# Kernel tuning notes

Hardware: AMD Instinct MI355X
Metric: run time of the kernel (lower is better)

The kernel has to match this reference:

```python
import jax, jax.numpy as jnp
import numpy as np

N_HEAD = 16
D_MODEL = 1024
BATCH = 2
SEQ = 2048


def setup_inputs() -> dict:
    key = jax.random.key(0)
    ks = jax.random.split(key, 12)
    s = 0.02
    inp = {
        "q": jax.random.normal(ks[0], (BATCH, SEQ, D_MODEL), jnp.float32),
        "k": jax.random.normal(ks[1], (BATCH, SEQ, D_MODEL), jnp.float32),
        "v": jax.random.normal(ks[2], (BATCH, SEQ, D_MODEL), jnp.float32),
        "Wq": jax.random.normal(ks[3], (D_MODEL, D_MODEL), jnp.float32) * s,
        "bq": jnp.zeros((D_MODEL,), jnp.float32),
        "Wk": jax.random.normal(ks[4], (D_MODEL, D_MODEL), jnp.float32) * s,
        "bk": jnp.zeros((D_MODEL,), jnp.float32),
        "Wv": jax.random.normal(ks[5], (D_MODEL, D_MODEL), jnp.float32) * s,
        "bv": jnp.zeros((D_MODEL,), jnp.float32),
        "Wo": jax.random.normal(ks[6], (D_MODEL, D_MODEL), jnp.float32) * s,
        "bo": jnp.zeros((D_MODEL,), jnp.float32),
    }
    return inp


def reference(q, k, v, Wq, bq, Wk, bk, Wv, bv, Wo, bo):
    B, S, D = q.shape
    H = N_HEAD
    Dh = D // H
    # NOTE: faithful to source -- scale uses d_model, not head_dim
    scale = D ** 0.5

    # torch nn.Linear: y = x @ W.T + b
    qw = q @ Wq.T + bq
    kw = k @ Wk.T + bk
    vw = v @ Wv.T + bv

    # chunk(n_head, dim=-1) == contiguous last-dim head slices
    qh = qw.reshape(B, S, H, Dh)
    kh = kw.reshape(B, S, H, Dh)
    vh = vw.reshape(B, S, H, Dh)

    scores = jnp.einsum("bshd,bthd->bhst", qh, kh) / scale  # [B,H,S,S]
    causal = jnp.triu(jnp.ones((S, S), dtype=bool), k=1)
    scores = jnp.where(causal, -jnp.inf, scores)
    p = jax.nn.softmax(scores, axis=-1)
    out = jnp.einsum("bhst,bthd->bshd", p, vh).reshape(B, S, D)
    return out @ Wo.T + bo
```

## Files before the change

### kernel.cpp

```cpp
#include <hip/hip_runtime.h>
#include <hip/hip_bf16.h>
#include <stdint.h>
#include <type_traits>

#define NHEAD  16
#define DMODEL 1024
#define BATCH  2
#define SEQ    2048
#define DH     64
#define MROWS  (BATCH*SEQ)

typedef __attribute__((ext_vector_type(8))) short bf16x8;
typedef __attribute__((ext_vector_type(4))) float f32x4;

__device__ inline short f2bs(float f) {
    __hip_bfloat16 h = __float2bfloat16(f);
    return *reinterpret_cast<short*>(&h);
}

__device__ inline uint32_t pk2f(float lo, float hi) {
    uint32_t ul, uh;
    __builtin_memcpy(&ul, &lo, 4);
    __builtin_memcpy(&uh, &hi, 4);
    return __builtin_amdgcn_perm(uh + 0x8000u, ul + 0x8000u, 0x07060302u);
}

__device__ inline float bs2f(short s) {
    const uint32_t u = (uint32_t)(uint16_t)s << 16;
    float f;
    __builtin_memcpy(&f, &u, 4);
    return f;
}

__device__ inline void async16(const void* g, void* l) {
    __builtin_amdgcn_global_load_lds(
        (__attribute__((address_space(1))) void*)g,
        (__attribute__((address_space(3))) void*)l, 16, 0, 0);
}

__global__ __launch_bounds__(256)
void convert_all(const float* __restrict__ Wq, const float* __restrict__ Wk,
                 const float* __restrict__ Wv, const float* __restrict__ Wo,
                 const float* __restrict__ q, const float* __restrict__ k,
                 const float* __restrict__ v,
                 __hip_bfloat16* __restrict__ Wqkv, __hip_bfloat16* __restrict__ Wob,
                 __hip_bfloat16* __restrict__ qb, __hip_bfloat16* __restrict__ kb,
                 __hip_bfloat16* __restrict__ vb)
{
    const int idx = (blockIdx.x * 256 + threadIdx.x) * 8;
    const float* src;
    __hip_bfloat16* dst;
    if (idx < 3 * 1048576) {
        const int g = idx >> 20;
        src = (g == 0 ? Wq : (g == 1 ? Wk : Wv)) + (idx & 1048575);
        dst = Wqkv + idx;
    } else if (idx < 4 * 1048576) {
        src = Wo + (idx - 3 * 1048576);
        dst = Wob + (idx - 3 * 1048576);
    } else if (idx < 8 * 1048576) {
        src = q + (idx - 4 * 1048576);
        dst = qb + (idx - 4 * 1048576);
    } else if (idx < 12 * 1048576) {
        src = k + (idx - 8 * 1048576);
        dst = kb + (idx - 8 * 1048576);
    } else {
        src = v + (idx - 12 * 1048576);
        dst = vb + (idx - 12 * 1048576);
    }
    float4 f0 = *(const float4*)src;
    float4 f1 = *(const float4*)(src + 4);
    short o[8];
    o[0] = f2bs(f0.x); o[1] = f2bs(f0.y); o[2] = f2bs(f0.z); o[3] = f2bs(f0.w);
    o[4] = f2bs(f1.x); o[5] = f2bs(f1.y); o[6] = f2bs(f1.z); o[7] = f2bs(f1.w);
    *(uint4*)dst = *(uint4*)o;
}

template <typename TC, bool DBUF, bool VTOUT>
__global__ __launch_bounds__(256, DBUF ? 2 : 3)
void gemm_bt(const __hip_bfloat16* __restrict__ A0, const __hip_bfloat16* __restrict__ A1,
             const __hip_bfloat16* __restrict__ A2,
             const __hip_bfloat16* __restrict__ B,
             const float* __restrict__ b0, const float* __restrict__ b1, const float* __restrict__ b2,
             TC* __restrict__ C0, TC* __restrict__ C1, TC* __restrict__ C2,
             float os0)
{
    __shared__ short As[DBUF ? 2 : 1][128 * 64];
    __shared__ short Bs[DBUF ? 2 : 1][128 * 64];

    const int t    = threadIdx.x;
    const int lane = t & 63;
    const int w    = t >> 6;
    const int wm   = (w >> 1) * 64;
    const int wn   = (w & 1) * 64;
    const int quad = lane >> 4;
    const int l16  = lane & 15;

    const int g = blockIdx.x >> 3;
    const __hip_bfloat16* A = (g == 0) ? A0 : (g == 1 ? A1 : A2);
    const float* bias       = (g == 0) ? b0 : (g == 1 ? b1 : b2);
    TC* C                   = (g == 0) ? C0 : (g == 1 ? C1 : C2);
    const float osc         = (g == 0) ? os0 : 1.f;
    const int    bm  = blockIdx.y * 128;
    const int    bnl = (blockIdx.x & 7) * 128;
    const size_t bng = (size_t)blockIdx.x * 128;

    f32x4 acc[4][4];
#pragma unroll
    for (int i = 0; i < 4; i++)
#pragma unroll
        for (int j = 0; j < 4; j++)
            acc[i][j] = (f32x4){0.f, 0.f, 0.f, 0.f};

    auto STAGEG = [&](int kt, int buf) {
#pragma unroll
        for (int i = 0; i < 4; i++) {
            const int p  = i * 256 + t;
            const int br = p >> 3;
            const int c8 = ((p & 7) - br) & 7;
            async16(B + (bng + br) * DMODEL + kt + c8 * 8,
                    &Bs[buf][(i * 256 + (w << 6)) * 8]);
            async16(A + (size_t)(bm + br) * DMODEL + kt + c8 * 8,
                    &As[buf][(i * 256 + (w << 6)) * 8]);
        }
    };

    int cur = 0;
    if constexpr (DBUF) STAGEG(0, 0);

    for (int kt = 0; kt < DMODEL; kt += 64) {
        __syncthreads();
        if constexpr (DBUF) {
            if (kt + 64 < DMODEL) STAGEG(kt + 64, cur ^ 1);
        } else {
            STAGEG(kt, 0);
            __syncthreads();
        }

#pragma unroll
        for (int kk = 0; kk < 2; kk++) {
            bf16x8 af[4], bf[4];
#pragma unroll
            for (int mi = 0; mi < 4; mi++) {
                const int row = wm + mi * 16 + l16;
                const int pc  = ((quad + 4 * kk) + row) & 7;
                af[mi] = *(const bf16x8*)&As[cur][row * 64 + pc * 8];
            }
#pragma unroll
            for (int ni = 0; ni < 4; ni++) {
                const int row = wn + ni * 16 + l16;
                const int pc  = ((quad + 4 * kk) + row) & 7;
                bf[ni] = *(const bf16x8*)&Bs[cur][row * 64 + pc * 8];
            }
#pragma unroll
            for (int mi = 0; mi < 4; mi++)
#pragma unroll
                for (int ni = 0; ni < 4; ni++)
                    acc[mi][ni] = __builtin_amdgcn_mfma_f32_16x16x32_bf16(
                        af[mi], bf[ni], acc[mi][ni], 0, 0, 0);
        }
        if constexpr (DBUF) cur ^= 1;
    }

#pragma unroll
    for (int mi = 0; mi < 4; mi++) {
#pragma unroll
        for (int ni = 0; ni < 4; ni++) {
            const int row0 = bm + wm + mi * 16 + quad * 4;
            const int coll = bnl + wn + ni * 16 + l16;
            const float bb = bias[coll];
            if (VTOUT && g == 2) {
                const int hh = coll >> 6, dd = coll & 63;
                const int bb_ = row0 >> 11, s0 = row0 & 2047;
                short o4[4];
#pragma unroll
                for (int r = 0; r < 4; r++) o4[r] = f2bs(acc[mi][ni][r] + bb);
                __hip_bfloat16* dst = (__hip_bfloat16*)C2 +
                    ((size_t)((bb_ * NHEAD + hh) * DH + dd)) * SEQ + s0;
                *(uint2*)dst = *(uint2*)o4;
            } else {
#pragma unroll
                for (int r = 0; r < 4; r++) {
                    const float val = (acc[mi][ni][r] + bb) * osc;
                    if constexpr (std::is_same<TC, float>::value)
                        C[(size_t)(row0 + r) * DMODEL + coll] = val;
                    else
                        C[(size_t)(row0 + r) * DMODEL + coll] = __float2bfloat16(val);
                }
            }
        }
    }
}

__global__ __launch_bounds__(256, 5)
void attn_flash_wg(const __hip_bfloat16* __restrict__ qp,
                   const __hip_bfloat16* __restrict__ kp,
                   const __hip_bfloat16* __restrict__ vt,
                   __hip_bfloat16* __restrict__ po0,
                   __hip_bfloat16* __restrict__ po1,
                   float* __restrict__ ml)
{
    __shared__ short Ks[2][64 * 64];
    __shared__ short Vs[2][64 * 64];

    const int t    = threadIdx.x;
    const int lane = t & 63;
    const int w    = t >> 6;
    const int l16  = lane & 15;
    const int quad = lane >> 4;

    const int bh   = blockIdx.x & 31;
    const int cidx = 79 - ((int)blockIdx.x >> 5);
    int st, c;
    if (cidx < 8)       { st = cidx; c = 0; }
    else if (cidx < 24) { const int u = cidx - 8;  st = 8 + (u >> 1); c = u & 1; }
    else if (cidx < 48) { const int u = cidx - 24; const int q3 = u / 3; st = 16 + q3; c = u - 3 * q3; }
    else                { const int u = cidx - 48; st = 24 + (u >> 2); c = u & 3; }
    const int bid = bh * 80 +
        ((st < 8) ? st : (st < 16) ? 8 + 2 * (st - 8) : (st < 24) ? 24 + 3 * (st - 16)
                                                      : 48 + 4 * (st - 24)) + c;
    const int b = bh >> 4;
    const int h = bh & 15;

    const __hip_bfloat16* qptr =
        qp + (size_t)(b * SEQ + 64 * st + 16 * w + l16) * DMODEL + h * DH + quad * 8;
    bf16x8 aq0 = *(const bf16x8*)qptr;
    bf16x8 aq1 = *(const bf16x8*)(qptr + 32);

    float l = 0.f;
    f32x4 oc[4];
#pragma unroll
    for (int dt = 0; dt < 4; dt++) oc[dt] = (f32x4){0.f, 0.f, 0.f, 0.f};

    const __hip_bfloat16* kbase = kp + (size_t)(b * SEQ) * DMODEL + h * DH;
    const __hip_bfloat16* vbase = vt + (size_t)(bh * DH) * SEQ;

    const int kmax   = 64 * st + 64;
    const int key_lo = 512 * c;
    const int nst    = (min(key_lo + 512, kmax) - key_lo) >> 6;
    const int rql    = 16 * w + l16;

    const int p1  = 256 + t;
    const int r0s = t >> 3,            r1s = p1 >> 3;
    const int c80 = ((t & 7) - r0s) & 7, c81 = ((p1 & 7) - r1s) & 7;
    const int kr0 = (r0s & 3) | ((r0s & 12) << 1) | ((r0s & 16) << 1) | ((r0s & 32) >> 3);
    const int kr1 = (r1s & 3) | ((r1s & 12) << 1) | ((r1s & 16) << 1) | ((r1s & 32) >> 3);
    const __hip_bfloat16* ks0 = kbase + (size_t)(key_lo + kr0) * DMODEL + c80 * 8;
    const __hip_bfloat16* ks1 = kbase + (size_t)(key_lo + kr1) * DMODEL + c81 * 8;
    const __hip_bfloat16* vs0 = vbase + (size_t)r0s * SEQ + key_lo + c80 * 8;
    const __hip_bfloat16* vs1 = vbase + (size_t)r1s * SEQ + key_lo + c81 * 8;

    const int d0 = ((w << 6)) * 8;
    const int d1 = (256 + (w << 6)) * 8;

    async16(ks0, &Ks[0][d0]);
    async16(ks1, &Ks[0][d1]);
    async16(vs0, &Vs[0][d0]);
    async16(vs1, &Vs[0][d1]);
    int cur = 0;
    int key0 = key_lo;

    for (int js = 0; js < nst; ++js) {
        __syncthreads();
        if (js + 1 < nst) {
            ks0 += (size_t)64 * DMODEL;  ks1 += (size_t)64 * DMODEL;
            vs0 += 64;                   vs1 += 64;
            const int nb = cur ^ 1;
            async16(ks0, &Ks[nb][d0]);
            async16(ks1, &Ks[nb][d1]);
            async16(vs0, &Vs[nb][d0]);
            async16(vs1, &Vs[nb][d1]);
        }

        f32x4 sc[4];
        __builtin_amdgcn_s_setprio(1);
#pragma unroll
        for (int ct = 0; ct < 4; ct++) {
            const int row = 16 * ct + l16;
            bf16x8 bk0 = *(const bf16x8*)&Ks[cur][row * 64 + ((quad + row) & 7) * 8];
            bf16x8 bk1 = *(const bf16x8*)&Ks[cur][row * 64 + ((quad + 4 + row) & 7) * 8];
            sc[ct] = __builtin_amdgcn_mfma_f32_16x16x32_bf16(
                bk0, aq0, (f32x4){0.f, 0.f, 0.f, 0.f}, 0, 0, 0);
            sc[ct] = __builtin_amdgcn_mfma_f32_16x16x32_bf16(bk1, aq1, sc[ct], 0, 0, 0);
        }
        __builtin_amdgcn_s_setprio(0);

        if (key0 == 64 * st) {
#pragma unroll
            for (int ct = 0; ct < 4; ct++)
#pragma unroll
                for (int r = 0; r < 4; r++) {
                    const int km = 8 * quad + 32 * (ct & 1) + 4 * (ct >> 1) + r;
                    if (km > rql) sc[ct][r] = -__builtin_inff();
                }
        }

        float psum = 0.f;
#pragma unroll
        for (int ct = 0; ct < 4; ct++)
#pragma unroll
            for (int r = 0; r < 4; r++) {
                const float e = exp2f(sc[ct][r]);
                sc[ct][r] = e;
                psum += e;
            }

        union U8 { uint32_t u[4]; bf16x8 v; } ap0u, ap1u;
        ap0u.u[0] = pk2f(sc[0][0], sc[0][1]);
        ap0u.u[1] = pk2f(sc[0][2], sc[0][3]);
        ap0u.u[2] = pk2f(sc[2][0], sc[2][1]);
        ap0u.u[3] = pk2f(sc[2][2], sc[2][3]);
        ap1u.u[0] = pk2f(sc[1][0], sc[1][1]);
        ap1u.u[1] = pk2f(sc[1][2], sc[1][3]);
        ap1u.u[2] = pk2f(sc[3][0], sc[3][1]);
        ap1u.u[3] = pk2f(sc[3][2], sc[3][3]);

        __builtin_amdgcn_s_setprio(1);
#pragma unroll
        for (int dt = 0; dt < 4; dt++) {
            const int row = 16 * dt + l16;
            bf16x8 bv0 = *(const bf16x8*)&Vs[cur][row * 64 + ((quad + row) & 7) * 8];
            bf16x8 bv1 = *(const bf16x8*)&Vs[cur][row * 64 + ((quad + 4 + row) & 7) * 8];
            oc[dt] = __builtin_amdgcn_mfma_f32_16x16x32_bf16(ap0u.v, bv0, oc[dt], 0, 0, 0);
            oc[dt] = __builtin_amdgcn_mfma_f32_16x16x32_bf16(ap1u.v, bv1, oc[dt], 0, 0, 0);
        }
        __builtin_amdgcn_s_setprio(0);

        psum += __shfl_xor(psum, 16);
        psum += __shfl_xor(psum, 32);
        l += psum;
        key0 += 64;
        cur ^= 1;
    }

    __hip_bfloat16* pp = (bid < 2048) ? po0 + (size_t)bid * 4096
                                      : po1 + (size_t)(bid - 2048) * 4096;
#pragma unroll
    for (int r = 0; r < 4; r++) {
        const int row = 16 * w + quad * 4 + r;
#pragma unroll
        for (int dt = 0; dt < 4; dt++)
            pp[row * 64 + 16 * dt + l16] = __float2bfloat16(oc[dt][r]);
    }
    if (quad == 0)
        ml[(size_t)bid * 64 + 16 * w + l16] = l;
}

__global__ __launch_bounds__(256)
void attn_reduce(const __hip_bfloat16* __restrict__ po0, const __hip_bfloat16* __restrict__ po1,
                 const float* __restrict__ ml, __hip_bfloat16* __restrict__ ao)
{
    const int t    = threadIdx.x;
    const int rh   = blockIdx.x & 1;
    const int st   = (blockIdx.x >> 1) & 31;
    const int bh   = blockIdx.x >> 6;
    const int nch  = (st >> 3) + 1;
    const int pre  = (st < 8) ? st : (st < 16) ? 8 + 2 * (st - 8)
                   : (st < 24) ? 24 + 3 * (st - 16) : 48 + 4 * (st - 24);
    const int bid0 = bh * 80 + pre;
    const int b    = bh >> 4;
    const int h    = bh & 15;
    const int row  = rh * 32 + (t >> 3);
    const int colg = (t & 7) * 8;

    float L = 0.f;
    float O[8];
#pragma unroll
    for (int j = 0; j < 8; j++) O[j] = 0.f;

    for (int cc = 0; cc < nch; cc++) {
        const int bidc = bid0 + cc;
        const __hip_bfloat16* pp = (bidc < 2048) ? po0 + (size_t)bidc * 4096
                                                 : po1 + (size_t)(bidc - 2048) * 4096;
        L += ml[(size_t)bidc * 64 + row];
        union { uint4 u; short s[8]; } pv;
        pv.u = *(const uint4*)&pp[row * 64 + colg];
#pragma unroll
        for (int j = 0; j < 8; j++) O[j] += bs2f(pv.s[j]);
    }
    const float inv = 1.f / L;
    short o8[8];
#pragma unroll
    for (int j = 0; j < 8; j++) o8[j] = f2bs(O[j] * inv);
    *(uint4*)&ao[(size_t)(b * SEQ + 64 * st + row) * DMODEL + h * DH + colg] = *(uint4*)o8;
}

extern "C" void kernel_launch(void* const* d_in, const int* in_sizes, int n_in,
                              void* d_out, int out_size, void* d_ws, size_t ws_size,
                              hipStream_t stream) {
    const float* q  = (const float*)d_in[0];
    const float* k  = (const float*)d_in[1];
    const float* v  = (const float*)d_in[2];
    const float* Wq = (const float*)d_in[3];
    const float* bq = (const float*)d_in[4];
    const float* Wk = (const float*)d_in[5];
    const float* bk = (const float*)d_in[6];
    const float* Wv = (const float*)d_in[7];
    const float* bv = (const float*)d_in[8];
    const float* Wo = (const float*)d_in[9];
    const float* bo = (const float*)d_in[10];
    float* out = (float*)d_out;

    __hip_bfloat16* Wqkv = (__hip_bfloat16*)d_ws;
    __hip_bfloat16* Wob  = Wqkv + (size_t)3072 * 1024;
    __hip_bfloat16* qp   = Wob  + (size_t)1024 * 1024;
    __hip_bfloat16* kp   = qp   + (size_t)MROWS * DMODEL;
    __hip_bfloat16* vtg  = kp   + (size_t)MROWS * DMODEL;
    __hip_bfloat16* vb   = vtg  + (size_t)MROWS * DMODEL;
    float*          mlb  = (float*)(vb + (size_t)MROWS * DMODEL);
    __hip_bfloat16* qb   = (__hip_bfloat16*)d_out;
    __hip_bfloat16* kb   = qb + (size_t)MROWS * DMODEL;
    __hip_bfloat16* ao   = vb;
    __hip_bfloat16* po0  = (__hip_bfloat16*)d_out;
    __hip_bfloat16* po1  = Wqkv;

    const float qscale = 0.03125f * 1.44269504088896340736f;

    hipLaunchKernelGGL(convert_all, dim3(8192), dim3(256), 0, stream,
                       Wq, Wk, Wv, Wo, q, k, v, Wqkv, Wob, qb, kb, vb);

    hipLaunchKernelGGL((gemm_bt<__hip_bfloat16, false, true>), dim3(24, 32), dim3(256), 0, stream,
                       qb, kb, vb, Wqkv, bq, bk, bv, qp, kp, vtg, qscale);

    hipLaunchKernelGGL(attn_flash_wg, dim3(2560), dim3(256), 0, stream,
                       qp, kp, vtg, po0, po1, mlb);

    hipLaunchKernelGGL(attn_reduce, dim3(2048), dim3(256), 0, stream,
                       po0, po1, mlb, ao);

    hipLaunchKernelGGL((gemm_bt<float, true, false>), dim3(8, 32), dim3(256), 0, stream,
                       ao, ao, ao, Wob, bo, bo, bo, out, out, out, 1.0f);
}
```

Baseline: 212.5 us.

## Drop split-KV chunking and reduce kernel; normalize attention output in place

Removes the key-range split (80 chunks per head) and the separate reduction kernel, so each workgroup handles a full causal query tile and writes the normalized bf16 output directly. Query tiles are mapped in a zig-zag order so that workgroups with long and short causal ranges are interleaved for load balance. This eliminates the partial-output writes, the reduction pass and one kernel launch. In exchange the grid shrinks to 1024 workgroups with very uneven per-workgroup work, which risks tail imbalance and lower occupancy.

```diff
diff --git a/kernel.cpp b/kernel.cpp
--- a/kernel.cpp
+++ b/kernel.cpp
@@ -23,13 +23,6 @@
     __builtin_memcpy(&ul, &lo, 4);
     __builtin_memcpy(&uh, &hi, 4);
     return __builtin_amdgcn_perm(uh + 0x8000u, ul + 0x8000u, 0x07060302u);
-}
-
-__device__ inline float bs2f(short s) {
-    const uint32_t u = (uint32_t)(uint16_t)s << 16;
-    float f;
-    __builtin_memcpy(&f, &u, 4);
-    return f;
 }
 
 __device__ inline void async16(const void* g, void* l) {
@@ -195,9 +188,7 @@
 void attn_flash_wg(const __hip_bfloat16* __restrict__ qp,
                    const __hip_bfloat16* __restrict__ kp,
                    const __hip_bfloat16* __restrict__ vt,
-                   __hip_bfloat16* __restrict__ po0,
-                   __hip_bfloat16* __restrict__ po1,
-                   float* __restrict__ ml)
+                   __hip_bfloat16* __restrict__ ao)
 {
     __shared__ short Ks[2][64 * 64];
     __shared__ short Vs[2][64 * 64];
@@ -208,16 +199,11 @@
     const int l16  = lane & 15;
     const int quad = lane >> 4;
 
-    const int bh   = blockIdx.x & 31;
-    const int cidx = 79 - ((int)blockIdx.x >> 5);
-    int st, c;
-    if (cidx < 8)       { st = cidx; c = 0; }
-    else if (cidx < 24) { const int u = cidx - 8;  st = 8 + (u >> 1); c = u & 1; }
-    else if (cidx < 48) { const int u = cidx - 24; const int q3 = u / 3; st = 16 + q3; c = u - 3 * q3; }
-    else                { const int u = cidx - 48; st = 24 + (u >> 2); c = u & 3; }
-    const int bid = bh * 80 +
-        ((st < 8) ? st : (st < 16) ? 8 + 2 * (st - 8) : (st < 24) ? 24 + 3 * (st - 16)
-                                                      : 48 + 4 * (st - 24)) + c;
+    const int bh = blockIdx.x & 31;
+    const int p  = blockIdx.x >> 5;
+    const int pa = p & 7, pb = p >> 3;
+    const int st = (pb == 0) ? pa : (pb == 1) ? 15 - pa
+                 : (pb == 2) ? 16 + pa : 31 - pa;
     const int b = bh >> 4;
     const int h = bh & 15;
 
@@ -234,20 +220,18 @@
     const __hip_bfloat16* kbase = kp + (size_t)(b * SEQ) * DMODEL + h * DH;
     const __hip_bfloat16* vbase = vt + (size_t)(bh * DH) * SEQ;
 
-    const int kmax   = 64 * st + 64;
-    const int key_lo = 512 * c;
-    const int nst    = (min(key_lo + 512, kmax) - key_lo) >> 6;
-    const int rql    = 16 * w + l16;
+    const int nst = st + 1;
+    const int rql = 16 * w + l16;
 
     const int p1  = 256 + t;
     const int r0s = t >> 3,            r1s = p1 >> 3;
     const int c80 = ((t & 7) - r0s) & 7, c81 = ((p1 & 7) - r1s) & 7;
     const int kr0 = (r0s & 3) | ((r0s & 12) << 1) | ((r0s & 16) << 1) | ((r0s & 32) >> 3);
     const int kr1 = (r1s & 3) | ((r1s & 12) << 1) | ((r1s & 16) << 1) | ((r1s & 32) >> 3);
-    const __hip_bfloat16* ks0 = kbase + (size_t)(key_lo + kr0) * DMODEL + c80 * 8;
-    const __hip_bfloat16* ks1 = kbase + (size_t)(key_lo + kr1) * DMODEL + c81 * 8;
-    const __hip_bfloat16* vs0 = vbase + (size_t)r0s * SEQ + key_lo + c80 * 8;
-    const __hip_bfloat16* vs1 = vbase + (size_t)r1s * SEQ + key_lo + c81 * 8;
+    const __hip_bfloat16* ks0 = kbase + (size_t)kr0 * DMODEL + c80 * 8;
+    const __hip_bfloat16* ks1 = kbase + (size_t)kr1 * DMODEL + c81 * 8;
+    const __hip_bfloat16* vs0 = vbase + (size_t)r0s * SEQ + c80 * 8;
+    const __hip_bfloat16* vs1 = vbase + (size_t)r1s * SEQ + c81 * 8;
 
     const int d0 = ((w << 6)) * 8;
     const int d1 = (256 + (w << 6)) * 8;
@@ -257,7 +241,7 @@
     async16(vs0, &Vs[0][d0]);
     async16(vs1, &Vs[0][d1]);
     int cur = 0;
-    int key0 = key_lo;
+    int key0 = 0;
 
     for (int js = 0; js < nst; ++js) {
         __syncthreads();
@@ -332,56 +316,16 @@
         cur ^= 1;
     }
 
-    __hip_bfloat16* pp = (bid < 2048) ? po0 + (size_t)bid * 4096
-                                      : po1 + (size_t)(bid - 2048) * 4096;
+    __hip_bfloat16* aobase = ao + (size_t)(b * SEQ + 64 * st + 16 * w) * DMODEL + h * DH;
 #pragma unroll
     for (int r = 0; r < 4; r++) {
-        const int row = 16 * w + quad * 4 + r;
+        const float lr  = __shfl(l, quad * 4 + r);
+        const float inv = 1.f / lr;
+        const int   row = quad * 4 + r;
 #pragma unroll
         for (int dt = 0; dt < 4; dt++)
-            pp[row * 64 + 16 * dt + l16] = __float2bfloat16(oc[dt][r]);
-    }
-    if (quad == 0)
-        ml[(size_t)bid * 64 + 16 * w + l16] = l;
-}
-
-__global__ __launch_bounds__(256)
-void attn_reduce(const __hip_bfloat16* __restrict__ po0, const __hip_bfloat16* __restrict__ po1,
-                 const float* __restrict__ ml, __hip_bfloat16* __restrict__ ao)
-{
-    const int t    = threadIdx.x;
-    const int rh   = blockIdx.x & 1;
-    const int st   = (blockIdx.x >> 1) & 31;
-    const int bh   = blockIdx.x >> 6;
-    const int nch  = (st >> 3) + 1;
-    const int pre  = (st < 8) ? st : (st < 16) ? 8 + 2 * (st - 8)
-                   : (st < 24) ? 24 + 3 * (st - 16) : 48 + 4 * (st - 24);
-    const int bid0 = bh * 80 + pre;
-    const int b    = bh >> 4;
-    const int h    = bh & 15;
-    const int row  = rh * 32 + (t >> 3);
-    const int colg = (t & 7) * 8;
-
-    float L = 0.f;
-    float O[8];
-#pragma unroll
-    for (int j = 0; j < 8; j++) O[j] = 0.f;
-
-    for (int cc = 0; cc < nch; cc++) {
-        const int bidc = bid0 + cc;
-        const __hip_bfloat16* pp = (bidc < 2048) ? po0 + (size_t)bidc * 4096
-                                                 : po1 + (size_t)(bidc - 2048) * 4096;
-        L += ml[(size_t)bidc * 64 + row];
-        union { uint4 u; short s[8]; } pv;
-        pv.u = *(const uint4*)&pp[row * 64 + colg];
-#pragma unroll
-        for (int j = 0; j < 8; j++) O[j] += bs2f(pv.s[j]);
-    }
-    const float inv = 1.f / L;
-    short o8[8];
-#pragma unroll
-    for (int j = 0; j < 8; j++) o8[j] = f2bs(O[j] * inv);
-    *(uint4*)&ao[(size_t)(b * SEQ + 64 * st + row) * DMODEL + h * DH + colg] = *(uint4*)o8;
+            aobase[(size_t)row * DMODEL + 16 * dt + l16] = __float2bfloat16(oc[dt][r] * inv);
+    }
 }
 
 extern "C" void kernel_launch(void* const* d_in, const int* in_sizes, int n_in,
@@ -406,12 +350,9 @@
     __hip_bfloat16* kp   = qp   + (size_t)MROWS * DMODEL;
     __hip_bfloat16* vtg  = kp   + (size_t)MROWS * DMODEL;
     __hip_bfloat16* vb   = vtg  + (size_t)MROWS * DMODEL;
-    float*          mlb  = (float*)(vb + (size_t)MROWS * DMODEL);
     __hip_bfloat16* qb   = (__hip_bfloat16*)d_out;
     __hip_bfloat16* kb   = qb + (size_t)MROWS * DMODEL;
     __hip_bfloat16* ao   = vb;
-    __hip_bfloat16* po0  = (__hip_bfloat16*)d_out;
-    __hip_bfloat16* po1  = Wqkv;
 
     const float qscale = 0.03125f * 1.44269504088896340736f;
 
@@ -421,11 +362,8 @@
     hipLaunchKernelGGL((gemm_bt<__hip_bfloat16, false, true>), dim3(24, 32), dim3(256), 0, stream,
                        qb, kb, vb, Wqkv, bq, bk, bv, qp, kp, vtg, qscale);
 
-    hipLaunchKernelGGL(attn_flash_wg, dim3(2560), dim3(256), 0, stream,
-                       qp, kp, vtg, po0, po1, mlb);
-
-    hipLaunchKernelGGL(attn_reduce, dim3(2048), dim3(256), 0, stream,
-                       po0, po1, mlb, ao);
+    hipLaunchKernelGGL(attn_flash_wg, dim3(1024), dim3(256), 0, stream,
+                       qp, kp, vtg, ao);
 
     hipLaunchKernelGGL((gemm_bt<float, true, false>), dim3(8, 32), dim3(256), 0, stream,
                        ao, ao, ao, Wob, bo, bo, bo, out, out, out, 1.0f);
```

Measured after the change: 211.3 us. Within noise of the previous version (-0.6%).
